# Kernel optimization log

Hardware: AMD Instinct MI355X
Metric: run time of the kernel (lower is better)

The kernel has to match this reference:

```python
import jax, jax.numpy as jnp
import numpy as np

VOCAB = 50000   # sum of sort/const/ind/conid/evar/fix/fixbody table sizes
STATE = 128
INIT = 2 * STATE  # treelstm packs (h, c) as one vector
OUT = 3
B, L = 256, 128


def setup_inputs() -> dict:
    key = jax.random.key(0)
    ks = jax.random.split(key, 8)
    ids = jax.random.randint(ks[0], (B, L), 0, VOCAB)
    embed_table = jax.random.normal(ks[1], (VOCAB, INIT), dtype=jnp.float32)
    # TreeLSTM whx: Linear(2*state, 5*state)
    whx_w = jax.random.normal(ks[2], (5 * STATE, 2 * STATE), dtype=jnp.float32) * (1.0 / np.sqrt(2 * STATE))
    whx_b = jnp.zeros((5 * STATE,), dtype=jnp.float32)
    init_state = jax.random.normal(ks[3], (1, INIT), dtype=jnp.float32)  # ast_cell_init_state
    final_w = jax.random.normal(ks[4], (OUT, STATE), dtype=jnp.float32) * (1.0 / np.sqrt(STATE))
    final_b = jnp.zeros((OUT,), dtype=jnp.float32)
    return {"ids": ids, "embed_table": embed_table, "whx_w": whx_w,
            "whx_b": whx_b, "init_state": init_state,
            "final_w": final_w, "final_b": final_b}


def _tree_lstm_step(hidden, x_t, whx_w, whx_b):
    # hidden: left (h, c) packed [B, 2S]; x_t: right (h, c) packed [B, 2S]
    right_h, right_c = jnp.split(x_t, 2, axis=-1)
    left_h, left_c = jnp.split(hidden, 2, axis=-1)
    z = jnp.concatenate([left_h, right_h], axis=-1) @ whx_w.T + whx_b  # [B, 5S]
    a, i, f1, f2, o = jnp.split(z, 5, axis=-1)
    c = jnp.tanh(a) * jax.nn.sigmoid(i) + jax.nn.sigmoid(f1) * left_c + jax.nn.sigmoid(f2) * right_c
    h = jax.nn.sigmoid(o) * jnp.tanh(c)
    return jnp.concatenate([h, c], axis=-1)


def reference(ids, embed_table, whx_w, whx_b, init_state, final_w, final_b):
    x = embed_table[ids]                         # [B, L, 2S] embedding lookup
    h0 = jnp.broadcast_to(init_state, (ids.shape[0], INIT))

    def step(hidden, x_t):
        return _tree_lstm_step(hidden, x_t, whx_w, whx_b), None

    hidden, _ = jax.lax.scan(step, h0, jnp.swapaxes(x, 0, 1))  # scan over L
    h = hidden[:, :STATE]                        # take h half of (h, c)
    return h @ final_w.T + final_b               # [B, outsize]
```

## Files before the change

kernel.cpp:

```cpp
#include <hip/hip_runtime.h>
#include <stdint.h>


constexpr int kL      = 128;
constexpr int kState  = 128;
constexpr int kInit   = 256;
constexpr int kRows   = 8;
constexpr int kBlocks = 32;
constexpr int kThreads= 512;
constexpr int kWElems = 5 * kState * kInit;
constexpr int kNTot   = 256 * kL;
constexpr int kZxCols = 5 * kState;
constexpr int kZRowB  = 2592;
constexpr int kRRowB  = 520;
constexpr int kZStep  = 256 * kZxCols * 4;

typedef __attribute__((ext_vector_type(8))) short short8;
typedef __attribute__((ext_vector_type(4))) short short4v;
typedef __attribute__((ext_vector_type(4))) float floatx4;

__device__ __forceinline__ uint16_t f2bf(float f) {
    union { float f; uint32_t i; } v; v.f = f;
    return (uint16_t)((v.i + 0x7FFFu + ((v.i >> 16) & 1u)) >> 16);
}
__device__ __forceinline__ float bf2f(uint16_t u) {
    union { uint32_t i; float f; } v; v.i = ((uint32_t)u) << 16; return v.f;
}
__device__ __forceinline__ float fexp2(float x) {
    return __builtin_amdgcn_exp2f(x);
}

#define GL16(SRC, LDSP, IMM) __builtin_amdgcn_global_load_lds(               \
    (const __attribute__((address_space(1))) uint32_t*)(uintptr_t)(SRC),     \
    (__attribute__((address_space(3))) uint32_t*)(uintptr_t)(LDSP), 16, (IMM), 0)
#define GL4(SRC, LDSP, IMM) __builtin_amdgcn_global_load_lds(                \
    (const __attribute__((address_space(1))) uint32_t*)(uintptr_t)(SRC),     \
    (__attribute__((address_space(3))) uint32_t*)(uintptr_t)(LDSP), 4, (IMM), 0)

__global__ __launch_bounds__(256)
void convert_weights_kernel(const float* __restrict__ wsrc,
                            uint16_t* __restrict__ wdst) {
    int i = blockIdx.x * 256 + threadIdx.x;
    float4 v = ((const float4*)wsrc)[i];
    uint16_t q[4] = { f2bf(v.x), f2bf(v.y), f2bf(v.z), f2bf(v.w) };
    ((short4v*)wdst)[i] = *(short4v*)q;
}

__global__ __launch_bounds__(256)
void zx_gemm_kernel(const uint16_t* __restrict__ wbf,
                    const float* __restrict__ embed,
                    const int* __restrict__ ids,
                    const float* __restrict__ whx_b,
                    float* __restrict__ zx)
{
    const int wv   = threadIdx.x >> 6;
    const int lane = threadIdx.x & 63;
    const int l15  = lane & 15;
    const int quad = lane >> 4;
    const int n0   = (blockIdx.x * 4 + wv) * 32;
    const int T    = n0 >> 8;
    const int B0   = (n0 & 255) + l15;
    const int id0  = ids[B0 * kL + T];
    const int id1  = ids[(B0 + 16) * kL + T];

    short8 xf0[4], xf1[4];
    const float* xr0 = embed + (size_t)id0 * kInit;
    const float* xr1 = embed + (size_t)id1 * kInit;
#pragma unroll
    for (int kk = 0; kk < 4; ++kk) {
        float4 a0 = *(const float4*)(xr0 + kk * 32 + quad * 8);
        float4 a1 = *(const float4*)(xr0 + kk * 32 + quad * 8 + 4);
        uint16_t qa[8] = { f2bf(a0.x), f2bf(a0.y), f2bf(a0.z), f2bf(a0.w),
                           f2bf(a1.x), f2bf(a1.y), f2bf(a1.z), f2bf(a1.w) };
        xf0[kk] = *(short8*)qa;
        float4 b0 = *(const float4*)(xr1 + kk * 32 + quad * 8);
        float4 b1 = *(const float4*)(xr1 + kk * 32 + quad * 8 + 4);
        uint16_t qb[8] = { f2bf(b0.x), f2bf(b0.y), f2bf(b0.z), f2bf(b0.w),
                           f2bf(b1.x), f2bf(b1.y), f2bf(b1.z), f2bf(b1.w) };
        xf1[kk] = *(short8*)qb;
    }

    float* zr0 = zx + (size_t)(n0 + l15) * kZxCols;
    float* zr1 = zx + (size_t)(n0 + 16 + l15) * kZxCols;
#pragma unroll 8
    for (int jf = 0; jf < 40; ++jf) {
        const uint16_t* wr = wbf + (size_t)(jf * 16 + l15) * kInit + kState;
        floatx4 bias = *(const floatx4*)(whx_b + jf * 16 + quad * 4);
        floatx4 acc0 = bias, acc1 = bias;
#pragma unroll
        for (int kk = 0; kk < 4; ++kk) {
            short8 wa = *(const short8*)(wr + kk * 32 + quad * 8);
            acc0 = __builtin_amdgcn_mfma_f32_16x16x32_bf16(wa, xf0[kk], acc0, 0, 0, 0);
            acc1 = __builtin_amdgcn_mfma_f32_16x16x32_bf16(wa, xf1[kk], acc1, 0, 0, 0);
        }
        __builtin_nontemporal_store(acc0, (floatx4*)(zr0 + jf * 16 + quad * 4));
        __builtin_nontemporal_store(acc1, (floatx4*)(zr1 + jf * 16 + quad * 4));
    }
}

__global__ __launch_bounds__(kThreads)
__attribute__((amdgpu_waves_per_eu(1, 2)))
void tree_lstm_kernel(const uint16_t* __restrict__ wbf,
                      const float* __restrict__ zx,
                      const float* __restrict__ embed,
                      const int* __restrict__ ids,
                      const float* __restrict__ init_state,
                      const float* __restrict__ final_w,
                      const float* __restrict__ final_b,
                      float* __restrict__ out)
{
    __shared__ alignas(16) uint8_t  zxt[3][kRows][kZRowB];
    __shared__ alignas(8)  uint8_t  rct[3][kRows][kRRowB];
    __shared__ alignas(16) uint16_t hb[2][16][kState];
    __shared__ float partial[kRows][3][4];

    const int tid  = threadIdx.x;
    const int w    = tid >> 6;
    const int lane = tid & 63;
    const int l15  = lane & 15;
    const int quad = lane >> 4;
    const int b0   = blockIdx.x * kRows;
    const int j0   = w * 16 + quad * 4;
    const int bl   = l15 & 7;
    const bool hig = l15 >= 8;
    const int jp   = j0 + (hig ? 2 : 0);
    const int wu   = __builtin_amdgcn_readfirstlane(w);
    const int irow = (b0 + wu) * kL;

    const int zx_rd = bl * kZRowB + j0 * 4;
    const int rc_rd = bl * kRRowB + jp * 4;

    uint8_t* zA = &zxt[0][0][0]; uint8_t* zB = &zxt[1][0][0]; uint8_t* zC = &zxt[2][0][0];
    uint8_t* rA = &rct[0][0][0]; uint8_t* rB = &rct[1][0][0]; uint8_t* rC = &rct[2][0][0];

    const char* zs16 = (const char*)zx + (size_t)(b0 + wu) * (kZxCols * 4) + lane * 16;
    const char* zs4  = (const char*)zx + (size_t)(b0 + wu) * (kZxCols * 4) + 2048 + lane * 4;

    short8 wf[5][4];
#pragma unroll
    for (int g = 0; g < 5; ++g) {
        const uint16_t* wrow = wbf + (size_t)(g * 128 + w * 16 + l15) * kInit;
#pragma unroll
        for (int kk = 0; kk < 4; ++kk)
            wf[g][kk] = *(const short8*)(wrow + kk * 32 + quad * 8);
    }

    const int g8   = 2 * w + (quad >> 1);
    const int hoff = (g8 ^ l15) * 8 + (quad & 1) * 4;
    float c_reg[2];
    {
        uint16_t h0[4];
#pragma unroll
        for (int r = 0; r < 4; ++r)
            h0[r] = f2bf(init_state[j0 + r]);
        c_reg[0] = init_state[128 + jp];
        c_reg[1] = init_state[128 + jp + 1];
        *(short4v*)&hb[0][l15][hoff] = *(short4v*)h0;
    }

    {
        uint8_t* zb0 = zA + w * kZRowB;
        GL16(zs16, zb0, 0);  GL16(zs16, zb0, 1024);
        GL4(zs4, zb0 + 2048, 0); GL4(zs4, zb0 + 2048, 256);
        int id0 = ids[irow + 0];
        const char* rs0 = (const char*)embed + (size_t)id0 * 1024 + 512 + lane * 4;
        uint8_t* rb0 = rA + w * kRRowB;
        GL4(rs0, rb0, 0); GL4(rs0, rb0, 256);
        zs16 += kZStep; zs4 += kZStep;
        uint8_t* zb1 = zB + w * kZRowB;
        GL16(zs16, zb1, 0);  GL16(zs16, zb1, 1024);
        GL4(zs4, zb1 + 2048, 0); GL4(zs4, zb1 + 2048, 256);
        int id1 = ids[irow + 1];
        const char* rs1 = (const char*)embed + (size_t)id1 * 1024 + 512 + lane * 4;
        uint8_t* rb1 = rB + w * kRRowB;
        GL4(rs1, rb1, 0); GL4(rs1, rb1, 256);
        zs16 += kZStep; zs4 += kZStep;
    }
    __syncthreads();

    const int eoff  = (quad & 1) * 4 + (hig ? 2 : 0);
    const int wlo   = (g8 ^ bl) * 8 + eoff;
    const int whi   = ((g8 ^ bl) ^ 8) * 8 + eoff;

    const float K1 = 1.442695041f;
    const float K2 = 2.885390082f;

#define GATE_CELL(RL, RCV, HVOUT)                                              \
    {                                                                          \
        float ga = hig ? acc[0][RL + 2] : acc[0][RL];                          \
        float gi = hig ? acc[1][RL + 2] : acc[1][RL];                          \
        float g1 = hig ? acc[2][RL + 2] : acc[2][RL];                          \
        float g2 = hig ? acc[3][RL + 2] : acc[3][RL];                          \
        float go = hig ? acc[4][RL + 2] : acc[4][RL];                          \
        float a  = fminf(ga, 15.f);                                            \
        float f1 = fminf(g1, 30.f);                                            \
        float f2 = fminf(g2, 30.f);                                            \
        float Ea = fexp2(a * K2);                                  \
        float Ei = fexp2(-gi * K1);                                \
        float P  = (Ea - 1.0f) *                                               \
            __builtin_amdgcn_rcpf((Ea + 1.0f) * (1.0f + Ei));                  \
        float E1 = fexp2(f1 * K1), E2 = fexp2(f2 * K1);                        \
        float lc = c_reg[RL], rc = (RCV);                                      \
        float num = E1 * (1.0f + E2) * lc + E2 * (1.0f + E1) * rc;             \
        float Q  = num * __builtin_amdgcn_rcpf((1.0f + E1) * (1.0f + E2));     \
        float c  = P + Q;                                                      \
        c_reg[RL] = c;                                                         \
        float Eo = fexp2(-go * K1);                                            \
        float cc = fminf(c, 15.f);                                             \
        float Ec = fexp2(cc * K2);                                             \
        float h  = (Ec - 1.0f) *                                               \
            __builtin_amdgcn_rcpf((1.0f + Eo) * (Ec + 1.0f));                  \
        HVOUT = f2bf(h);                                                       \
    }

#define LSTM_STEP(T, CUR, NXT, ZRD, RRD, ZWR, RWR)                             \
    {                                                                          \
         \
        const uint8_t* zrow = (ZRD) + zx_rd;                                   \
        floatx4 acc[5];                                                        \
        _Pragma("unroll")                                                      \
        for (int g = 0; g < 5; ++g)                                            \
            acc[g] = *(const floatx4*)(zrow + g * 512);                        \
        float2 rcv = *(const float2*)((RRD) + rc_rd);                          \
        const uint16_t* hrow = &hb[CUR][l15][0];                               \
        short8 xf0 = *(const short8*)(hrow + ((0 * 4 + quad) ^ l15) * 8);      \
        short8 xf1 = *(const short8*)(hrow + ((1 * 4 + quad) ^ l15) * 8);      \
        short8 xf2 = *(const short8*)(hrow + ((2 * 4 + quad) ^ l15) * 8);      \
        short8 xf3 = *(const short8*)(hrow + ((3 * 4 + quad) ^ l15) * 8);      \
                  \
        int tn2 = (T) + 2; if (tn2 > kL - 1) tn2 = kL - 1;                     \
        uint8_t* zwb = (ZWR) + w * kZRowB;                                     \
        GL16(zs16, zwb, 0);                                                    \
        GL16(zs16, zwb, 1024);                                                 \
        GL4(zs4, zwb + 2048, 0);                                               \
        GL4(zs4, zwb + 2048, 256);                                             \
        int idn = ids[irow + tn2];                                             \
        const char* rsn = (const char*)embed + (size_t)idn * 1024 + 512        \
                          + lane * 4;                                          \
        uint8_t* rwb = (RWR) + w * kRRowB;                                     \
        GL4(rsn, rwb, 0);                                                      \
        GL4(rsn, rwb, 256);                                                    \
        size_t adv = ((T) + 3 <= kL - 1) ? (size_t)kZStep : 0;                 \
        zs16 += adv; zs4 += adv;                                               \
                                                  \
        _Pragma("unroll")                                                      \
        for (int g = 0; g < 5; ++g)                                            \
            acc[g] = __builtin_amdgcn_mfma_f32_16x16x32_bf16(wf[g][0], xf0, acc[g], 0, 0, 0); \
        _Pragma("unroll")                                                      \
        for (int g = 0; g < 5; ++g)                                            \
            acc[g] = __builtin_amdgcn_mfma_f32_16x16x32_bf16(wf[g][1], xf1, acc[g], 0, 0, 0); \
        _Pragma("unroll")                                                      \
        for (int g = 0; g < 5; ++g)                                            \
            acc[g] = __builtin_amdgcn_mfma_f32_16x16x32_bf16(wf[g][2], xf2, acc[g], 0, 0, 0); \
        _Pragma("unroll")                                                      \
        for (int g = 0; g < 5; ++g)                                            \
            acc[g] = __builtin_amdgcn_mfma_f32_16x16x32_bf16(wf[g][3], xf3, acc[g], 0, 0, 0); \
                                                     \
        uint16_t hv0, hv1;                                                     \
        GATE_CELL(0, rcv.x, hv0)                                               \
        GATE_CELL(1, rcv.y, hv1)                                               \
        uint32_t hp = (uint32_t)hv0 | ((uint32_t)hv1 << 16);                   \
        *(uint32_t*)&hb[NXT][bl][wlo]     = hp;                                \
        *(uint32_t*)&hb[NXT][bl + 8][whi] = hp;                                \
              \
        asm volatile("s_waitcnt vmcnt(6) lgkmcnt(0)" ::: "memory");            \
        __builtin_amdgcn_sched_barrier(0);                                     \
        __builtin_amdgcn_s_barrier();                                          \
        __builtin_amdgcn_sched_barrier(0);                                     \
    }

#pragma unroll 1
    for (int t2 = 0; t2 < kL; t2 += 2) {
        LSTM_STEP(t2,     0, 1, zA, rA, zC, rC)
        LSTM_STEP(t2 + 1, 1, 0, zB, rB, zA, rA)
        uint8_t* tz = zA; zA = zC; zC = zB; zB = tz;
        uint8_t* tr = rA; rA = rC; rC = rB; rB = tr;
    }
#undef LSTM_STEP
#undef GATE_CELL

    if (tid < kRows * 12) {
        int b = tid / 12, rem = tid % 12;
        int o = rem >> 2, q4 = rem & 3;
        float s = 0.f;
        const float* wrow = final_w + o * kState;
#pragma unroll 8
        for (int j = q4 * 32; j < q4 * 32 + 32; ++j) {
            uint16_t hval = hb[0][b][((j >> 3) ^ b) * 8 + (j & 7)];
            s += bf2f(hval) * wrow[j];
        }
        partial[b][o][q4] = s;
    }
    __syncthreads();
    if (tid < kRows * 3) {
        int b = tid / 3, o = tid % 3;
        float s = partial[b][o][0] + partial[b][o][1] +
                  partial[b][o][2] + partial[b][o][3] + final_b[o];
        out[(b0 + b) * 3 + o] = s;
    }
}

extern "C" void kernel_launch(void* const* d_in, const int* in_sizes, int n_in,
                              void* d_out, int out_size, void* d_ws, size_t ws_size,
                              hipStream_t stream) {
    const int*   ids        = (const int*)d_in[0];
    const float* embed      = (const float*)d_in[1];
    const float* whx_w      = (const float*)d_in[2];
    const float* whx_b      = (const float*)d_in[3];
    const float* init_state = (const float*)d_in[4];
    const float* final_w    = (const float*)d_in[5];
    const float* final_b    = (const float*)d_in[6];
    float*       out        = (float*)d_out;
    uint16_t*    wbf        = (uint16_t*)d_ws;
    float*       zx         = (float*)((char*)d_ws + (size_t)kWElems * 2);

    convert_weights_kernel<<<kWElems / 4 / 256, 256, 0, stream>>>(whx_w, wbf);
    zx_gemm_kernel<<<kNTot / 128, 256, 0, stream>>>(wbf, embed, ids, whx_b, zx);
    tree_lstm_kernel<<<kBlocks, kThreads, 0, stream>>>(
        wbf, zx, embed, ids, init_state, final_w, final_b, out);
}
```

Measured before the change: 242.6 us.

## Fuse weight bf16 conversion into GEMM and LSTM kernels, stage weights in LDS

Removes the separate weight-conversion kernel and its launch. The zx GEMM now converts the right half of whx_w to bf16 itself and stores it in swizzled LDS, with each block covering one timestep and half the gate columns. The recurrent kernel converts its register-resident weight fragments from fp32 at load. This saves a launch and a global round trip, at the cost of each GEMM block redoing a 320x128 conversion and more fp32 weight traffic.

```diff
diff --git a/kernel.cpp b/kernel.cpp
--- a/kernel.cpp
+++ b/kernel.cpp
@@ -8,7 +8,6 @@
 constexpr int kRows   = 8;
 constexpr int kBlocks = 32;
 constexpr int kThreads= 512;
-constexpr int kWElems = 5 * kState * kInit;
 constexpr int kNTot   = 256 * kL;
 constexpr int kZxCols = 5 * kState;
 constexpr int kZRowB  = 2592;
@@ -37,70 +36,84 @@
     (const __attribute__((address_space(1))) uint32_t*)(uintptr_t)(SRC),     \
     (__attribute__((address_space(3))) uint32_t*)(uintptr_t)(LDSP), 4, (IMM), 0)
 
-__global__ __launch_bounds__(256)
-void convert_weights_kernel(const float* __restrict__ wsrc,
-                            uint16_t* __restrict__ wdst) {
-    int i = blockIdx.x * 256 + threadIdx.x;
-    float4 v = ((const float4*)wsrc)[i];
-    uint16_t q[4] = { f2bf(v.x), f2bf(v.y), f2bf(v.z), f2bf(v.w) };
-    ((short4v*)wdst)[i] = *(short4v*)q;
-}
-
-__global__ __launch_bounds__(256)
-void zx_gemm_kernel(const uint16_t* __restrict__ wbf,
+__global__ __launch_bounds__(512)
+void zx_gemm_kernel(const float* __restrict__ whx_w,
                     const float* __restrict__ embed,
                     const int* __restrict__ ids,
                     const float* __restrict__ whx_b,
                     float* __restrict__ zx)
 {
-    const int wv   = threadIdx.x >> 6;
-    const int lane = threadIdx.x & 63;
-    const int l15  = lane & 15;
-    const int quad = lane >> 4;
-    const int n0   = (blockIdx.x * 4 + wv) * 32;
-    const int T    = n0 >> 8;
-    const int B0   = (n0 & 255) + l15;
-    const int id0  = ids[B0 * kL + T];
-    const int id1  = ids[(B0 + 16) * kL + T];
-
+    __shared__ alignas(16) uint16_t wl[320 * 128];
+
+    const int tid   = threadIdx.x;
+    const int wv    = tid >> 6;
+    const int lane  = tid & 63;
+    const int l15   = lane & 15;
+    const int quad  = lane >> 4;
+    const int jhalf = blockIdx.x & 1;
+    const int nblk  = blockIdx.x >> 1;
+
+    const int n0  = nblk * 256 + wv * 32;
+    const int T   = nblk;
+    const int B0  = wv * 32 + l15;
+    const int id0 = ids[B0 * kL + T];
+    const int id1 = ids[(B0 + 16) * kL + T];
     short8 xf0[4], xf1[4];
-    const float* xr0 = embed + (size_t)id0 * kInit;
-    const float* xr1 = embed + (size_t)id1 * kInit;
-#pragma unroll
-    for (int kk = 0; kk < 4; ++kk) {
-        float4 a0 = *(const float4*)(xr0 + kk * 32 + quad * 8);
-        float4 a1 = *(const float4*)(xr0 + kk * 32 + quad * 8 + 4);
-        uint16_t qa[8] = { f2bf(a0.x), f2bf(a0.y), f2bf(a0.z), f2bf(a0.w),
-                           f2bf(a1.x), f2bf(a1.y), f2bf(a1.z), f2bf(a1.w) };
-        xf0[kk] = *(short8*)qa;
-        float4 b0 = *(const float4*)(xr1 + kk * 32 + quad * 8);
-        float4 b1 = *(const float4*)(xr1 + kk * 32 + quad * 8 + 4);
-        uint16_t qb[8] = { f2bf(b0.x), f2bf(b0.y), f2bf(b0.z), f2bf(b0.w),
-                           f2bf(b1.x), f2bf(b1.y), f2bf(b1.z), f2bf(b1.w) };
-        xf1[kk] = *(short8*)qb;
-    }
-
-    float* zr0 = zx + (size_t)(n0 + l15) * kZxCols;
-    float* zr1 = zx + (size_t)(n0 + 16 + l15) * kZxCols;
-#pragma unroll 8
-    for (int jf = 0; jf < 40; ++jf) {
-        const uint16_t* wr = wbf + (size_t)(jf * 16 + l15) * kInit + kState;
-        floatx4 bias = *(const floatx4*)(whx_b + jf * 16 + quad * 4);
+    {
+        const float* xr0 = embed + (size_t)id0 * kInit;
+        const float* xr1 = embed + (size_t)id1 * kInit;
+#pragma unroll
+        for (int kk = 0; kk < 4; ++kk) {
+            float4 a0 = *(const float4*)(xr0 + kk * 32 + quad * 8);
+            float4 a1 = *(const float4*)(xr0 + kk * 32 + quad * 8 + 4);
+            uint16_t qa[8] = { f2bf(a0.x), f2bf(a0.y), f2bf(a0.z), f2bf(a0.w),
+                               f2bf(a1.x), f2bf(a1.y), f2bf(a1.z), f2bf(a1.w) };
+            xf0[kk] = *(short8*)qa;
+            float4 b0 = *(const float4*)(xr1 + kk * 32 + quad * 8);
+            float4 b1 = *(const float4*)(xr1 + kk * 32 + quad * 8 + 4);
+            uint16_t qb[8] = { f2bf(b0.x), f2bf(b0.y), f2bf(b0.z), f2bf(b0.w),
+                               f2bf(b1.x), f2bf(b1.y), f2bf(b1.z), f2bf(b1.w) };
+            xf1[kk] = *(short8*)qb;
+        }
+    }
+
+#pragma unroll
+    for (int t = 0; t < 10; ++t) {
+        int c   = t * 512 + tid;
+        int jl  = c >> 4;
+        int c16 = c & 15;
+        const float* src = whx_w
+            + (size_t)(jhalf * 320 + jl) * kInit + kState + c16 * 8;
+        float4 v0 = *(const float4*)(src);
+        float4 v1 = *(const float4*)(src + 4);
+        uint16_t q[8] = { f2bf(v0.x), f2bf(v0.y), f2bf(v0.z), f2bf(v0.w),
+                          f2bf(v1.x), f2bf(v1.y), f2bf(v1.z), f2bf(v1.w) };
+        *(short8*)&wl[jl * 128 + ((c16 ^ (jl & 7)) * 8)] = *(short8*)q;
+    }
+    __syncthreads();
+
+    float* zr0 = zx + (size_t)(n0 + l15) * kZxCols + jhalf * 320;
+    float* zr1 = zx + (size_t)(n0 + 16 + l15) * kZxCols + jhalf * 320;
+#pragma unroll 5
+    for (int jfl = 0; jfl < 20; ++jfl) {
+        const uint16_t* base = wl + (size_t)(jfl * 16 + l15) * 128;
+        floatx4 bias = *(const floatx4*)(whx_b + jhalf * 320 + jfl * 16 + quad * 4);
         floatx4 acc0 = bias, acc1 = bias;
 #pragma unroll
         for (int kk = 0; kk < 4; ++kk) {
-            short8 wa = *(const short8*)(wr + kk * 32 + quad * 8);
+            int ch = (kk * 4 + quad) ^ (l15 & 7);
+            short8 wa = *(const short8*)(base + ch * 8);
             acc0 = __builtin_amdgcn_mfma_f32_16x16x32_bf16(wa, xf0[kk], acc0, 0, 0, 0);
             acc1 = __builtin_amdgcn_mfma_f32_16x16x32_bf16(wa, xf1[kk], acc1, 0, 0, 0);
         }
-        __builtin_nontemporal_store(acc0, (floatx4*)(zr0 + jf * 16 + quad * 4));
-        __builtin_nontemporal_store(acc1, (floatx4*)(zr1 + jf * 16 + quad * 4));
+        __builtin_nontemporal_store(acc0, (floatx4*)(zr0 + jfl * 16 + quad * 4));
+        __builtin_nontemporal_store(acc1, (floatx4*)(zr1 + jfl * 16 + quad * 4));
     }
 }
 
 __global__ __launch_bounds__(kThreads)
 __attribute__((amdgpu_waves_per_eu(1, 2)))
-void tree_lstm_kernel(const uint16_t* __restrict__ wbf,
+void tree_lstm_kernel(const float* __restrict__ whx_w,
                       const float* __restrict__ zx,
                       const float* __restrict__ embed,
                       const int* __restrict__ ids,
@@ -139,10 +152,15 @@
     short8 wf[5][4];
 #pragma unroll
     for (int g = 0; g < 5; ++g) {
-        const uint16_t* wrow = wbf + (size_t)(g * 128 + w * 16 + l15) * kInit;
-#pragma unroll
-        for (int kk = 0; kk < 4; ++kk)
-            wf[g][kk] = *(const short8*)(wrow + kk * 32 + quad * 8);
+        const float* wrow = whx_w + (size_t)(g * 128 + w * 16 + l15) * kInit;
+#pragma unroll
+        for (int kk = 0; kk < 4; ++kk) {
+            float4 a = *(const float4*)(wrow + kk * 32 + quad * 8);
+            float4 b = *(const float4*)(wrow + kk * 32 + quad * 8 + 4);
+            uint16_t q[8] = { f2bf(a.x), f2bf(a.y), f2bf(a.z), f2bf(a.w),
+                              f2bf(b.x), f2bf(b.y), f2bf(b.z), f2bf(b.w) };
+            wf[g][kk] = *(short8*)q;
+        }
     }
 
     const int g8   = 2 * w + (quad >> 1);
@@ -311,11 +329,9 @@
     const float* final_w    = (const float*)d_in[5];
     const float* final_b    = (const float*)d_in[6];
     float*       out        = (float*)d_out;
-    uint16_t*    wbf        = (uint16_t*)d_ws;
-    float*       zx         = (float*)((char*)d_ws + (size_t)kWElems * 2);
-
-    convert_weights_kernel<<<kWElems / 4 / 256, 256, 0, stream>>>(whx_w, wbf);
-    zx_gemm_kernel<<<kNTot / 128, 256, 0, stream>>>(wbf, embed, ids, whx_b, zx);
+    float*       zx         = (float*)d_ws;
+
+    zx_gemm_kernel<<<256, 512, 0, stream>>>(whx_w, embed, ids, whx_b, zx);
     tree_lstm_kernel<<<kBlocks, kThreads, 0, stream>>>(
-        wbf, zx, embed, ids, init_state, final_w, final_b, out);
-}
+        whx_w, zx, embed, ids, init_state, final_w, final_b, out);
+}
```

New measurement: 236.9 us. 2.4% less time.
